# Performance work log

Measured on AMD Instinct MI355X. Metric: run time of the kernel, lower is better.

The kernel has to match this reference:

```python
import jax, jax.numpy as jnp
import numpy as np

H = 16; KV = 4; D = 128; HID = 2048; MAX_POS = 4096; RANK = 8; ALPHA = 16.0; THETA = 10000.0


def _lora_dense(x, kernel, a, b):
    # base kernel path is stop-gradient'd in the original LoRADense
    x = x.astype(jnp.bfloat16)
    y = x @ jax.lax.stop_gradient(kernel.astype(jnp.bfloat16))
    y = y + (ALPHA / RANK) * ((x @ a.astype(jnp.bfloat16)) @ b.astype(jnp.bfloat16))
    return y.astype(jnp.float32)


def _apply_rope(xq, xk, position_ids):
    # complex rotation expressed with real cos/sin on interleaved (even, odd) pairs
    dt = xq.dtype
    xq = xq.astype(jnp.bfloat16).astype(jnp.float32)
    xk = xk.astype(jnp.bfloat16).astype(jnp.float32)
    d = xq.shape[-1]
    inv_freq = 1.0 / THETA ** (jnp.arange(0, d, 2)[: d // 2].astype(jnp.float32) / d)
    angles = jnp.arange(MAX_POS, dtype=jnp.float32)[:, None] * inv_freq[None, :]  # (max_pos, d/2)
    cos = jnp.cos(angles)[position_ids][:, :, None, :]  # (b, s, 1, d/2)
    sin = jnp.sin(angles)[position_ids][:, :, None, :]

    def rot(x):
        xe = x[..., 0::2]
        xo = x[..., 1::2]
        re = xe * cos - xo * sin
        im = xe * sin + xo * cos
        return jnp.stack((re, im), axis=-1).reshape(x.shape)

    return rot(xq).astype(dt), rot(xk).astype(dt)


def _forward(hidden_states, attention_mask, position_ids, wq_kernel, wq_a, wq_b,
             wk_kernel, wk_a, wk_b, wv_kernel, wv_a, wv_b, wo_kernel, wo_a, wo_b):
    b, s, _ = hidden_states.shape
    hs = hidden_states.astype(jnp.bfloat16)
    xq = _lora_dense(hs, wq_kernel, wq_a, wq_b).reshape(b, s, H, D)
    g = H // KV
    # GQA: repeat each kv head g times along the head axis ('b s (h d) -> b s (h g) d')
    xk = jnp.repeat(_lora_dense(hs, wk_kernel, wk_a, wk_b).reshape(b, s, KV, D), g, axis=2)
    xv = jnp.repeat(_lora_dense(hs, wv_kernel, wv_a, wv_b).reshape(b, s, KV, D), g, axis=2)
    xq, xk = _apply_rope(xq, xk, position_ids)
    causal = jnp.tril(jnp.ones((s, s), dtype=bool))
    mask = attention_mask[:, None, None, :] & causal[None, None]  # (b, 1, q, k)
    bias = jnp.where(mask, 0.0, jnp.finfo(jnp.float32).min)
    scale = 1.0 / np.sqrt(D).astype(np.float32)
    scores = jnp.einsum('bqhd,bkhd->bhqk', (xq * scale).astype(jnp.bfloat16),
                        xk.astype(jnp.bfloat16)).astype(jnp.float32) + bias
    attn = jax.nn.softmax(scores, axis=-1)
    out = jnp.einsum('bhqk,bkhd->bqhd', attn, xv).reshape(b, s, H * D)
    return _lora_dense(out, wo_kernel, wo_a, wo_b)


def setup_inputs():
    key = jax.random.key(0)
    ks = jax.random.split(key, 16)
    B, S = 2, 2048
    w = lambda k, shp, sc=0.02: jax.random.normal(k, shp, dtype=jnp.float32) * sc
    return {
        'hidden_states': jax.random.normal(ks[0], (B, S, HID), dtype=jnp.float32),
        'attention_mask': jnp.ones((B, S), dtype=bool),
        'position_ids': jnp.broadcast_to(jnp.arange(S, dtype=jnp.int32), (B, S)),
        'wq_kernel': w(ks[1], (HID, H * D)),
        'wq_a': w(ks[2], (HID, RANK), 0.01),
        'wq_b': w(ks[3], (RANK, H * D), 0.01),
        'wk_kernel': w(ks[4], (HID, KV * D)),
        'wk_a': w(ks[5], (HID, RANK), 0.01),
        'wk_b': w(ks[6], (RANK, KV * D), 0.01),
        'wv_kernel': w(ks[7], (HID, KV * D)),
        'wv_a': w(ks[8], (HID, RANK), 0.01),
        'wv_b': w(ks[9], (RANK, KV * D), 0.01),
        'wo_kernel': w(ks[10], (H * D, HID)),
        'wo_a': w(ks[11], (H * D, RANK), 0.01),
        'wo_b': w(ks[12], (RANK, HID), 0.01),
    }


def reference(hidden_states, attention_mask, position_ids, wq_kernel, wq_a, wq_b,
              wk_kernel, wk_a, wk_b, wv_kernel, wv_a, wv_b, wo_kernel, wo_a, wo_b):
    return _forward(hidden_states, attention_mask, position_ids, wq_kernel, wq_a, wq_b,
                    wk_kernel, wk_a, wk_b, wv_kernel, wv_a, wv_b, wo_kernel, wo_a, wo_b)
```

## Files before the change

### kernel.cpp

```cpp
#include <hip/hip_runtime.h>
#include <hip/hip_bf16.h>
#include <cstdint>

#define H_    16
#define KV_   4
#define D_    128
#define HID_  2048
#define B_    2
#define S_    2048
#define NROW_ (B_*S_)
#define HD_   (H_*D_)
#define KVD_  (KV_*D_)
#define NQKV_ (HD_ + 2*KVD_)
#define SCALE_ 0.08838834764831843f
#define L2E_   1.44269504088896f
#define QSC_   (SCALE_ * L2E_)
#define THR2_  11.5415603f
#define NEG_  -1e30f

typedef float  f32x4  __attribute__((ext_vector_type(4)));
typedef __bf16 bf16x8 __attribute__((ext_vector_type(8)));
typedef __bf16 bf16x4 __attribute__((ext_vector_type(4)));

__device__ __forceinline__ unsigned short f2bf(float x) {
  unsigned u = __float_as_uint(x);
  return (unsigned short)((u + 0x7FFFu + ((u >> 16) & 1u)) >> 16);
}
__device__ __forceinline__ float bf2f(unsigned short h) {
  return __uint_as_float(((unsigned)h) << 16);
}

__device__ __forceinline__ void glds16(const void* g, void* l) {
  typedef __attribute__((address_space(1))) const char G;
  typedef __attribute__((address_space(3))) char L;
  __builtin_amdgcn_global_load_lds((const G*)(unsigned long long)g,
                                   (L*)(unsigned)(unsigned long long)l, 16, 0, 0);
}

__global__ __launch_bounds__(256) void fold_all(
    const float* __restrict__ wq, const float* __restrict__ wqa, const float* __restrict__ wqb,
    const float* __restrict__ wk, const float* __restrict__ wka, const float* __restrict__ wkb,
    const float* __restrict__ wv, const float* __restrict__ wva, const float* __restrict__ wvb,
    const float* __restrict__ wo, const float* __restrict__ woa, const float* __restrict__ wob,
    unsigned short* __restrict__ Wqkv, unsigned short* __restrict__ Wot,
    const float* __restrict__ hs, unsigned short* __restrict__ Xb,
    float* __restrict__ tab) {
  const int z = blockIdx.z;
  const int tid = threadIdx.x;
  if (z == 4) {
    int lin = blockIdx.y * 32 + blockIdx.x;
    size_t base = (size_t)lin * 2048 + tid * 8;
#pragma unroll
    for (int i = 0; i < 8; ++i) {
      float4 v = ((const float4*)hs)[base + i];
      ushort4 o; o.x = f2bf(v.x); o.y = f2bf(v.y); o.z = f2bf(v.z); o.w = f2bf(v.w);
      ((ushort4*)Xb)[base + i] = o;
    }
    return;
  }
  if (z == 5) {
    int lin = blockIdx.y * 32 + blockIdx.x;
    if (lin >= 512) return;
    int p = lin * 4 + (tid >> 6);
    int j = tid & 63;
    float invf = __powf(10000.0f, -(float)j / 64.0f);
    float a = (float)p * invf;
    float s, c;
    sincosf(a, &s, &c);
    tab[(p * 64 + j) * 2 + 0] = c;
    tab[(p * 64 + j) * 2 + 1] = s;
    return;
  }
  const float *W, *A, *Bm; unsigned short* Wt; int N;
  if (z == 0)      { W = wq; A = wqa; Bm = wqb; Wt = Wqkv;                         N = 2048; }
  else if (z == 1) { W = wk; A = wka; Bm = wkb; Wt = Wqkv + (size_t)2048 * 2048;   N = 512;  }
  else if (z == 2) { W = wv; A = wva; Bm = wvb; Wt = Wqkv + (size_t)2560 * 2048;   N = 512;  }
  else             { W = wo; A = woa; Bm = wob; Wt = Wot;                          N = 2048; }
  const int K = 2048;
  const int k0 = blockIdx.x << 6, n0 = blockIdx.y << 6;
  if (n0 >= N) return;

  __shared__ float Bs[8 * 64];
  __shared__ unsigned short tt[64 * 72];
#pragma unroll
  for (int i = 0; i < 2; ++i) {
    int c = i * 256 + tid;
    Bs[c] = bf2f(f2bf(Bm[(c >> 6) * N + n0 + (c & 63)]));
  }
  __syncthreads();
  const int kr = tid >> 2, nc = (tid & 3) << 4;
  float a[8];
#pragma unroll
  for (int r = 0; r < 8; ++r) a[r] = 2.0f * bf2f(f2bf(A[(k0 + kr) * 8 + r]));
#pragma unroll
  for (int i = 0; i < 4; ++i) {
    float4 wv4 = *(const float4*)(W + (size_t)(k0 + kr) * N + n0 + nc + i * 4);
    float e[4] = {wv4.x, wv4.y, wv4.z, wv4.w};
#pragma unroll
    for (int q = 0; q < 4; ++q) {
      int n = nc + i * 4 + q;
      float acc = bf2f(f2bf(e[q]));
#pragma unroll
      for (int r = 0; r < 8; ++r) acc += a[r] * Bs[r * 64 + n];
      tt[kr * 72 + n] = f2bf(acc);
    }
  }
  __syncthreads();
  const int nr = tid >> 2, kc = (tid & 3) << 4;
#pragma unroll
  for (int i = 0; i < 2; ++i) {
    unsigned short o[8];
#pragma unroll
    for (int e2 = 0; e2 < 8; ++e2) o[e2] = tt[(kc + i * 8 + e2) * 72 + nr];
    *(bf16x8*)(Wt + (size_t)(n0 + nr) * K + k0 + kc + i * 8) = *(const bf16x8*)o;
  }
}

__global__ __launch_bounds__(256) void ropevt(unsigned short* __restrict__ QKV,
                                              const int* __restrict__ pos,
                                              const float* __restrict__ trig,
                                              unsigned short* __restrict__ VT) {
  __shared__ unsigned short t[64 * 65];
  const int bx = blockIdx.x, tid = threadIdx.x;
  if (bx < 2560) {
    int gid = bx * 256 + tid;
    int row = gid / 160;
    int ch = gid - row * 160;
    bool isq = ch < 128;
    int col = isq ? (ch << 4) : (HD_ + ((ch - 128) << 4));
    int j0 = (isq ? (ch & 7) : ((ch - 128) & 7)) << 3;
    int pp = pos[row];
    const float* tb = trig + ((size_t)pp * 64 + j0) * 2;
    float4 t0 = *(const float4*)(tb);
    float4 t1 = *(const float4*)(tb + 4);
    float4 t2 = *(const float4*)(tb + 8);
    float4 t3 = *(const float4*)(tb + 12);
    float cc[8] = {t0.x, t0.z, t1.x, t1.z, t2.x, t2.z, t3.x, t3.z};
    float ss[8] = {t0.y, t0.w, t1.y, t1.w, t2.y, t2.w, t3.y, t3.w};
    unsigned short* base = QKV + (size_t)row * NQKV_ + col;
    unsigned short xin[16], xo[16];
    *(bf16x8*)xin = *(const bf16x8*)base;
    *(bf16x8*)(xin + 8) = *(const bf16x8*)(base + 8);
    float scl = isq ? QSC_ : 1.0f;
#pragma unroll
    for (int p = 0; p < 8; ++p) {
      float x0 = bf2f(xin[2 * p]), x1 = bf2f(xin[2 * p + 1]);
      float re = (x0 * cc[p] - x1 * ss[p]) * scl;
      float im = (x0 * ss[p] + x1 * cc[p]) * scl;
      xo[2 * p] = f2bf(re); xo[2 * p + 1] = f2bf(im);
    }
    *(bf16x8*)base = *(const bf16x8*)xo;
    *(bf16x8*)(base + 8) = *(const bf16x8*)(xo + 8);
  } else {
    const int bb = bx - 2560;
    const int s0 = (bb & 31) << 6, d0 = ((bb >> 5) & 1) << 6;
    const int bk = bb >> 6, b = bk >> 2, hkv = bk & 3;
#pragma unroll
    for (int i = 0; i < 2; ++i) {
      int c = i * 256 + tid;
      int sr = c >> 3, c8 = c & 7;
      bf16x8 v = *(const bf16x8*)(QKV + (size_t)(b * S_ + s0 + sr) * NQKV_
                                  + HD_ + KVD_ + hkv * D_ + d0 + c8 * 8);
      const unsigned short* u = (const unsigned short*)&v;
#pragma unroll
      for (int k = 0; k < 8; ++k) t[sr * 65 + c8 * 8 + k] = u[k];
    }
    __syncthreads();
#pragma unroll
    for (int i = 0; i < 2; ++i) {
      int c = i * 256 + tid;
      int dr = c >> 3, c8 = c & 7;
      unsigned short o[8];
#pragma unroll
      for (int k = 0; k < 8; ++k) o[k] = t[(c8 * 8 + k) * 65 + dr];
      *(bf16x8*)(VT + ((size_t)(bk * 128 + d0 + dr)) * S_ + s0 + c8 * 8) =
          *(const bf16x8*)o;
    }
  }
}

template <int BN, int OUTF32>
__global__ __launch_bounds__(512, 1) void gemm8p(const unsigned short* __restrict__ A,
                                                 const unsigned short* __restrict__ Bt,
                                                 void* __restrict__ C,
                                                 int M, int N, int K) {
  constexpr int ASLAB = 256 * 64;
  constexpr int BSLAB = BN * 64;
  constexpr int NFR = BN / 64;
  constexpr int WCOL = BN / 4;
  __shared__ __align__(16) unsigned short lds[3 * ASLAB + 2 * BSLAB];
  unsigned short* const ldsB = lds + 3 * ASLAB;
  const int tid = threadIdx.x, lane = tid & 63, w = tid >> 6;
  const int g = lane >> 4, l15 = lane & 15;
  const int wm = w >> 2, wn = w & 3;

  const int x = blockIdx.x & 7, inner = blockIdx.x >> 3;
  const int bm = (x >> 1) * 4 + (inner >> 3);
  const int bn = (x & 1) * 8 + (inner & 7);
  const int row0 = bm << 8, col0 = bn * BN;
  const int nkt = K >> 6;

  auto stA = [&](int kt, int slab, int part) {
    if (kt < nkt) {
#pragma unroll
      for (int j = 0; j < 2; ++j) {
        int jj = part * 2 + j;
        int c = jj * 512 + tid;
        int r = c >> 3, s = c & 7, slot = s ^ (r & 7);
        glds16(A + (size_t)(row0 + r) * K + (kt << 6) + slot * 8,
               (char*)(lds + slab * ASLAB) + (size_t)(jj * 512 + w * 64) * 16);
      }
    }
  };
  auto stB = [&](int kt, int slab, int part) {
    if (kt < nkt) {
      constexpr int split = (NFR == 3) ? 2 : 1;
      const int jlo = part ? split : 0;
      const int jhi = part ? NFR : split;
#pragma unroll
      for (int jj = 0; jj < NFR; ++jj) {
        if (jj >= jlo && jj < jhi) {
          int c = jj * 512 + tid;
          int r = c >> 3, s = c & 7, slot = s ^ (r & 7);
          glds16(Bt + (size_t)(col0 + r) * K + (kt << 6) + slot * 8,
                 (char*)(ldsB + slab * BSLAB) + (size_t)(jj * 512 + w * 64) * 16);
        }
      }
    }
  };

  f32x4 acc[8][NFR];
#pragma unroll
  for (int i = 0; i < 8; ++i)
#pragma unroll
    for (int j = 0; j < NFR; ++j) acc[i][j] = (f32x4){0.f, 0.f, 0.f, 0.f};
  bf16x8 bfr[NFR][2];

  stB(0, 0, 0); stB(0, 0, 1);
  stA(0, 0, 0); stA(0, 0, 1);
  stA(1, 1, 0); stA(1, 1, 1);
  asm volatile("s_waitcnt vmcnt(0)" ::: "memory");
  __builtin_amdgcn_s_barrier();

  int am = 0;
  for (int kt = 0; kt < nkt; ++kt) {
    const unsigned short* bufA = lds + am * ASLAB;
    const unsigned short* bufB = ldsB + (kt & 1) * BSLAB;
    int as2 = am + 2; if (as2 >= 3) as2 -= 3;
    const int bs1 = (kt + 1) & 1;
#pragma unroll
    for (int q = 0; q < 4; ++q) {
      bf16x8 af[2][2];
#pragma unroll
      for (int mi = 0; mi < 2; ++mi) {
        int r = wm * 128 + q * 32 + mi * 16 + l15;
#pragma unroll
        for (int ks = 0; ks < 2; ++ks) {
          int slot = (ks * 4 + g) ^ (r & 7);
          af[mi][ks] = *(const bf16x8*)(bufA + r * 64 + slot * 8);
        }
      }
      if (q == 0) {
#pragma unroll
        for (int ni = 0; ni < NFR; ++ni) {
          int r = wn * WCOL + ni * 16 + l15;
#pragma unroll
          for (int ks = 0; ks < 2; ++ks) {
            int slot = (ks * 4 + g) ^ (r & 7);
            bfr[ni][ks] = *(const bf16x8*)(bufB + r * 64 + slot * 8);
          }
        }
      }
      if (q == 0)      stB(kt + 1, bs1, 0);
      else if (q == 1) stB(kt + 1, bs1, 1);
      else if (q == 2) stA(kt + 2, as2, 0);
      else {
        stA(kt + 2, as2, 1);
        if (kt + 2 < nkt) asm volatile("s_waitcnt vmcnt(4)" ::: "memory");
        else              asm volatile("s_waitcnt vmcnt(0)" ::: "memory");
      }
      __builtin_amdgcn_s_barrier();
      asm volatile("s_waitcnt lgkmcnt(0)" ::: "memory");
      __builtin_amdgcn_s_setprio(1);
#pragma unroll
      for (int ks = 0; ks < 2; ++ks)
#pragma unroll
        for (int mi = 0; mi < 2; ++mi)
#pragma unroll
          for (int ni = 0; ni < NFR; ++ni)
            acc[q * 2 + mi][ni] =
                __builtin_amdgcn_mfma_f32_16x16x32_bf16(af[mi][ks], bfr[ni][ks],
                                                        acc[q * 2 + mi][ni], 0, 0, 0);
      __builtin_amdgcn_s_setprio(0);
      __builtin_amdgcn_s_barrier();
    }
    am = (am + 1 == 3) ? 0 : am + 1;
  }

#pragma unroll
  for (int f = 0; f < 8; ++f)
#pragma unroll
    for (int jj = 0; jj < 4; ++jj) {
      int r = row0 + wm * 128 + f * 16 + g * 4 + jj;
#pragma unroll
      for (int ni = 0; ni < NFR; ++ni) {
        int cc = col0 + wn * WCOL + ni * 16 + l15;
        float v = acc[f][ni][jj];
        if (OUTF32) ((float*)C)[(size_t)r * N + cc] = v;
        else        ((unsigned short*)C)[(size_t)r * N + cc] = f2bf(v);
      }
    }
}

__global__ __launch_bounds__(512, 4) void attn_k(const unsigned short* __restrict__ QKV,
                                                 const unsigned short* __restrict__ VT,
                                                 unsigned short* __restrict__ O) {
  __shared__ __align__(16) unsigned short smem[32768];
  const int tid = threadIdx.x, lane = tid & 63, w = tid >> 6;
  const int g = lane >> 4, l15 = lane & 15;
  const int wr = w & 1;
  const int wh = w >> 1;

  const int dd = blockIdx.x;
  const int grp = dd & 7;
  const int b = grp >> 2, hkv = grp & 3;
  const int qt = 63 - (dd >> 3);
  const int q_base = qt << 5;
  const int ntile = (qt >> 1) + 1;
  const int h = hkv * 4 + wh;

  const unsigned short* QKVk0 = QKV + (size_t)b * S_ * NQKV_ + HD_ + hkv * D_;
  const unsigned short* VT0  = VT + (size_t)(b * 4 + hkv) * 128 * S_;

  int gk[2], gv[2], dsl[2];
#pragma unroll
  for (int i = 0; i < 2; ++i) {
    int c = i * 512 + tid;
    { int r = c >> 4, s = c & 15; gk[i] = r * NQKV_ + (s ^ (r & 7)) * 8; }
    { int d = c >> 3, s = c & 7;  gv[i] = d * S_ + (s ^ (d & 7)) * 8; }
    dsl[i] = (i * 512 + w * 64) * 16;
  }
  int koff[4][4], voff[2][8], pwo[4], pro[2];
#pragma unroll
  for (int ks = 0; ks < 4; ++ks)
#pragma unroll
    for (int m = 0; m < 4; ++m) {
      int r = m * 16 + l15;
      koff[ks][m] = r * 128 + ((ks * 4 + g) ^ (r & 7)) * 8;
    }
#pragma unroll
  for (int ks = 0; ks < 2; ++ks)
#pragma unroll
    for (int nd = 0; nd < 8; ++nd) {
      int d = nd * 16 + l15;
      voff[ks][nd] = d * 64 + ((ks * 4 + g) ^ (d & 7)) * 8;
    }
#pragma unroll
  for (int m = 0; m < 4; ++m)
    pwo[m] = l15 * 64 + ((2 * m + (g >> 1) + l15) & 7) * 8 + (g & 1) * 4;
#pragma unroll
  for (int ks = 0; ks < 2; ++ks)
    pro[ks] = l15 * 64 + ((ks * 4 + g + l15) & 7) * 8;
  const int PB = 24576 + w * 1024;
  char* const smemc = (char*)smem;
  const int qg = q_base + wr * 16 + l15;

#define STAGEKV(KB, VOB) do {                                               \
    const unsigned short* bk_ = QKVk0 + (size_t)(KB) * NQKV_;               \
    const unsigned short* bv_ = VT0 + (KB);                                 \
    _Pragma("unroll")                                                       \
    for (int i_ = 0; i_ < 2; ++i_) {                                        \
      glds16(bk_ + gk[i_], smemc + dsl[i_]);                                \
      glds16(bv_ + gv[i_], smemc + (VOB) + dsl[i_]);                        \
    }                                                                       \
  } while (0)

#define QKT(SACC) do {                                                      \
    _Pragma("unroll") for (int m = 0; m < 4; ++m)                           \
      SACC[m] = (f32x4){0.f, 0.f, 0.f, 0.f};                                \
    __builtin_amdgcn_s_setprio(1);                                          \
    _Pragma("unroll") for (int ks = 0; ks < 4; ++ks) {                      \
      bf16x8 kf[4];                                                         \
      _Pragma("unroll") for (int m = 0; m < 4; ++m)                         \
        kf[m] = *(const bf16x8*)(smem + koff[ks][m]);                       \
      _Pragma("unroll") for (int m = 0; m < 4; ++m)                         \
        SACC[m] = __builtin_amdgcn_mfma_f32_16x16x32_bf16(kf[m], qf[ks], SACC[m], 0, 0, 0); \
    }                                                                       \
    __builtin_amdgcn_s_setprio(0);                                          \
  } while (0)

#define SOFTPV(SACC, VOHS, TCUR) do {                                       \
    if ((TCUR) == ntile - 1) {                                              \
      const int kb_ = (TCUR) << 6;                                          \
      _Pragma("unroll") for (int m = 0; m < 4; ++m)                         \
        _Pragma("unroll") for (int jj = 0; jj < 4; ++jj)                    \
          if (kb_ + m * 16 + g * 4 + jj > qg) SACC[m][jj] = NEG_;           \
    }                                                                       \
    float pm = NEG_;                                                        \
    _Pragma("unroll") for (int m = 0; m < 4; ++m)                           \
      _Pragma("unroll") for (int jj = 0; jj < 4; ++jj)                      \
        pm = fmaxf(pm, SACC[m][jj]);                                        \
    bool skip = __all(pm <= mrun + THR2_);                                  \
    float mnew;                                                             \
    if (skip) {                                                             \
      mnew = mrun;                                                          \
    } else {                                                                \
      pm = fmaxf(pm, __shfl_xor(pm, 16));                                   \
      pm = fmaxf(pm, __shfl_xor(pm, 32));                                   \
      mnew = fmaxf(mrun, pm);                                               \
    }                                                                       \
    float ls = 0.f;                                                         \
    _Pragma("unroll") for (int m = 0; m < 4; ++m)                           \
      _Pragma("unroll") for (int jj = 0; jj < 4; ++jj) {                    \
        float pv = __builtin_amdgcn_exp2f(SACC[m][jj] - mnew);              \
        SACC[m][jj] = pv;                                                   \
        ls += pv;                                                           \
      }                                                                     \
    _Pragma("unroll") for (int m = 0; m < 4; ++m) {                         \
      bf16x4 pk = {(__bf16)SACC[m][0], (__bf16)SACC[m][1],                  \
                   (__bf16)SACC[m][2], (__bf16)SACC[m][3]};                 \
      *(bf16x4*)(smem + PB + pwo[m]) = pk;                                  \
    }                                                                       \
    if (skip) {                                                             \
      lrun += ls;                                                           \
    } else {                                                                \
      float sc = __builtin_amdgcn_exp2f(mrun - mnew);                       \
      lrun = lrun * sc + ls;                                                \
      mrun = mnew;                                                          \
      _Pragma("unroll") for (int jj = 0; jj < 4; ++jj) {                    \
        int srcl = (lane & 48) | (g * 4 + jj);                              \
        float s = __shfl(sc, srcl);                                         \
        _Pragma("unroll") for (int nd = 0; nd < 8; ++nd) oacc[nd][jj] *= s; \
      }                                                                     \
    }                                                                       \
    __builtin_amdgcn_s_setprio(1);                                          \
    _Pragma("unroll") for (int ks = 0; ks < 2; ++ks) {                      \
      bf16x8 pf = *(const bf16x8*)(smem + PB + pro[ks]);                    \
      _Pragma("unroll") for (int nd = 0; nd < 8; ++nd) {                    \
        bf16x8 vf = *(const bf16x8*)(smem + (VOHS) + voff[ks][nd]);         \
        oacc[nd] = __builtin_amdgcn_mfma_f32_16x16x32_bf16(pf, vf, oacc[nd], 0, 0, 0); \
      }                                                                     \
    }                                                                       \
    __builtin_amdgcn_s_setprio(0);                                          \
  } while (0)

  bf16x8 qf[4];
#pragma unroll
  for (int ks = 0; ks < 4; ++ks)
    qf[ks] = *(const bf16x8*)(QKV + (size_t)(b * S_ + qg) * NQKV_
                              + h * D_ + ks * 32 + g * 8);

  f32x4 oacc[8];
#pragma unroll
  for (int nd = 0; nd < 8; ++nd) oacc[nd] = (f32x4){0.f, 0.f, 0.f, 0.f};
  float mrun = NEG_, lrun = 0.f;

  STAGEKV(0, 16384);
  __syncthreads();
  for (int t = 0; t < ntile; t += 2) {
    {
      f32x4 sacc[4];
      QKT(sacc);
      __syncthreads();
      if (t + 1 < ntile) STAGEKV((t + 1) << 6, 32768);
      SOFTPV(sacc, 8192, t);
      __syncthreads();
    }
    if (t + 1 >= ntile) break;
    {
      f32x4 sacc[4];
      QKT(sacc);
      __syncthreads();
      if (t + 2 < ntile) STAGEKV((t + 2) << 6, 16384);
      SOFTPV(sacc, 16384, t + 1);
      __syncthreads();
    }
  }

  lrun += __shfl_xor(lrun, 16);
  lrun += __shfl_xor(lrun, 32);

  float inv[4];
#pragma unroll
  for (int jj = 0; jj < 4; ++jj) {
    int srcl = (lane & 48) | (g * 4 + jj);
    inv[jj] = 1.0f / __shfl(lrun, srcl);
  }
  unsigned short* sE = smem + wh * 4352;
#pragma unroll
  for (int nd = 0; nd < 8; ++nd)
#pragma unroll
    for (int jj = 0; jj < 4; ++jj) {
      __bf16 e = (__bf16)(oacc[nd][jj] * inv[jj]);
      sE[(wr * 16 + g * 4 + jj) * 136 + nd * 16 + l15] = *(unsigned short*)&e;
    }
  __syncthreads();
#pragma unroll
  for (int i = 0; i < 4; ++i) {
    int c = i * 512 + tid;
    int hh2 = c >> 9, r = (c >> 4) & 31, c16 = c & 15;
    bf16x8 vv = *(const bf16x8*)(smem + hh2 * 4352 + r * 136 + c16 * 8);
    *(bf16x8*)(O + (size_t)(b * S_ + q_base + r) * HD_ + (hkv * 4 + hh2) * D_ + c16 * 8) = vv;
  }
#undef STAGEKV
#undef QKT
#undef SOFTPV
}

extern "C" void kernel_launch(void* const* d_in, const int* in_sizes, int n_in,
                              void* d_out, int out_size, void* d_ws, size_t ws_size,
                              hipStream_t stream) {
  const float* hs  = (const float*)d_in[0];
  const int*   pos = (const int*)d_in[2];
  const float* wq  = (const float*)d_in[3];
  const float* wqa = (const float*)d_in[4];
  const float* wqb = (const float*)d_in[5];
  const float* wk  = (const float*)d_in[6];
  const float* wka = (const float*)d_in[7];
  const float* wkb = (const float*)d_in[8];
  const float* wv  = (const float*)d_in[9];
  const float* wva = (const float*)d_in[10];
  const float* wvb = (const float*)d_in[11];
  const float* wo  = (const float*)d_in[12];
  const float* woa = (const float*)d_in[13];
  const float* wob = (const float*)d_in[14];

  char* ws = (char*)d_ws;
  unsigned short* Xb   = (unsigned short*)(ws);
  unsigned short* Wqkv = (unsigned short*)(ws + 16777216);
  unsigned short* Wot  = (unsigned short*)(ws + 29360128);
  unsigned short* QKV  = (unsigned short*)(ws + 37748736);
  unsigned short* VT   = (unsigned short*)(ws + 62914560);
  float*          trig = (float*)(ws + 67108864);

  fold_all<<<dim3(32, 32, 6), 256, 0, stream>>>(wq, wqa, wqb, wk, wka, wkb,
                                                wv, wva, wvb, wo, woa, wob,
                                                Wqkv, Wot, hs, Xb, trig);
  gemm8p<192, 0><<<256, 512, 0, stream>>>(Xb, Wqkv, QKV, 4096, 3072, 2048);
  ropevt<<<3072, 256, 0, stream>>>(QKV, pos, trig, VT);
  attn_k<<<512, 512, 0, stream>>>(QKV, VT, Xb );
  gemm8p<128, 1><<<256, 512, 0, stream>>>(Xb, Wot, d_out, 4096, 2048, 2048);
}
```

Baseline: 189.0 us.

## Give each attention wave two 16-row query slabs to reuse K/V fragments

The attention kernel drops from 8 waves per block to 4. Each wave now handles one head and both 16-row query sub-tiles, so every K and V fragment read from shared memory feeds two MFMAs instead of one. The main loop is restructured to process one tile per iteration with alternating buffers, and per-row softmax state is doubled. This cuts LDS read traffic per MFMA, at the cost of more registers per thread and fewer waves to hide latency.

```diff
diff --git a/kernel.cpp b/kernel.cpp
--- a/kernel.cpp
+++ b/kernel.cpp
@@ -312,14 +312,12 @@
     }
 }
 
-__global__ __launch_bounds__(512, 4) void attn_k(const unsigned short* __restrict__ QKV,
+__global__ __launch_bounds__(256, 2) void attn_k(const unsigned short* __restrict__ QKV,
                                                  const unsigned short* __restrict__ VT,
                                                  unsigned short* __restrict__ O) {
   __shared__ __align__(16) unsigned short smem[32768];
   const int tid = threadIdx.x, lane = tid & 63, w = tid >> 6;
   const int g = lane >> 4, l15 = lane & 15;
-  const int wr = w & 1;
-  const int wh = w >> 1;
 
   const int dd = blockIdx.x;
   const int grp = dd & 7;
@@ -327,20 +325,20 @@
   const int qt = 63 - (dd >> 3);
   const int q_base = qt << 5;
   const int ntile = (qt >> 1) + 1;
-  const int h = hkv * 4 + wh;
+  const int h = hkv * 4 + w;
 
   const unsigned short* QKVk0 = QKV + (size_t)b * S_ * NQKV_ + HD_ + hkv * D_;
   const unsigned short* VT0  = VT + (size_t)(b * 4 + hkv) * 128 * S_;
 
-  int gk[2], gv[2], dsl[2];
-#pragma unroll
-  for (int i = 0; i < 2; ++i) {
-    int c = i * 512 + tid;
+  int gk[4], gv[4], dsl[4];
+#pragma unroll
+  for (int i = 0; i < 4; ++i) {
+    int c = i * 256 + tid;
     { int r = c >> 4, s = c & 15; gk[i] = r * NQKV_ + (s ^ (r & 7)) * 8; }
     { int d = c >> 3, s = c & 7;  gv[i] = d * S_ + (s ^ (d & 7)) * 8; }
-    dsl[i] = (i * 512 + w * 64) * 16;
-  }
-  int koff[4][4], voff[2][8], pwo[4], pro[2];
+    dsl[i] = (i * 256 + w * 64) * 16;
+  }
+  int koff[4][4], voff[2][8], pwo[2][4], pro[2][2];
 #pragma unroll
   for (int ks = 0; ks < 4; ++ks)
 #pragma unroll
@@ -356,155 +354,178 @@
       voff[ks][nd] = d * 64 + ((ks * 4 + g) ^ (d & 7)) * 8;
     }
 #pragma unroll
-  for (int m = 0; m < 4; ++m)
-    pwo[m] = l15 * 64 + ((2 * m + (g >> 1) + l15) & 7) * 8 + (g & 1) * 4;
-#pragma unroll
-  for (int ks = 0; ks < 2; ++ks)
-    pro[ks] = l15 * 64 + ((ks * 4 + g + l15) & 7) * 8;
-  const int PB = 24576 + w * 1024;
+  for (int n = 0; n < 2; ++n)
+#pragma unroll
+    for (int m = 0; m < 4; ++m)
+      pwo[n][m] = (n * 16 + l15) * 64 + ((2 * m + (g >> 1) + l15) & 7) * 8 + (g & 1) * 4;
+#pragma unroll
+  for (int mq = 0; mq < 2; ++mq)
+#pragma unroll
+    for (int ks = 0; ks < 2; ++ks)
+      pro[mq][ks] = (mq * 16 + l15) * 64 + ((ks * 4 + g + l15) & 7) * 8;
+  const int PB = 24576 + w * 2048;
   char* const smemc = (char*)smem;
-  const int qg = q_base + wr * 16 + l15;
 
 #define STAGEKV(KB, VOB) do {                                               \
     const unsigned short* bk_ = QKVk0 + (size_t)(KB) * NQKV_;               \
     const unsigned short* bv_ = VT0 + (KB);                                 \
     _Pragma("unroll")                                                       \
-    for (int i_ = 0; i_ < 2; ++i_) {                                        \
+    for (int i_ = 0; i_ < 4; ++i_) {                                        \
       glds16(bk_ + gk[i_], smemc + dsl[i_]);                                \
       glds16(bv_ + gv[i_], smemc + (VOB) + dsl[i_]);                        \
     }                                                                       \
   } while (0)
 
-#define QKT(SACC) do {                                                      \
-    _Pragma("unroll") for (int m = 0; m < 4; ++m)                           \
-      SACC[m] = (f32x4){0.f, 0.f, 0.f, 0.f};                                \
-    __builtin_amdgcn_s_setprio(1);                                          \
-    _Pragma("unroll") for (int ks = 0; ks < 4; ++ks) {                      \
-      bf16x8 kf[4];                                                         \
-      _Pragma("unroll") for (int m = 0; m < 4; ++m)                         \
-        kf[m] = *(const bf16x8*)(smem + koff[ks][m]);                       \
-      _Pragma("unroll") for (int m = 0; m < 4; ++m)                         \
-        SACC[m] = __builtin_amdgcn_mfma_f32_16x16x32_bf16(kf[m], qf[ks], SACC[m], 0, 0, 0); \
-    }                                                                       \
-    __builtin_amdgcn_s_setprio(0);                                          \
-  } while (0)
-
-#define SOFTPV(SACC, VOHS, TCUR) do {                                       \
-    if ((TCUR) == ntile - 1) {                                              \
-      const int kb_ = (TCUR) << 6;                                          \
-      _Pragma("unroll") for (int m = 0; m < 4; ++m)                         \
-        _Pragma("unroll") for (int jj = 0; jj < 4; ++jj)                    \
-          if (kb_ + m * 16 + g * 4 + jj > qg) SACC[m][jj] = NEG_;           \
-    }                                                                       \
-    float pm = NEG_;                                                        \
-    _Pragma("unroll") for (int m = 0; m < 4; ++m)                           \
-      _Pragma("unroll") for (int jj = 0; jj < 4; ++jj)                      \
-        pm = fmaxf(pm, SACC[m][jj]);                                        \
-    bool skip = __all(pm <= mrun + THR2_);                                  \
-    float mnew;                                                             \
-    if (skip) {                                                             \
-      mnew = mrun;                                                          \
-    } else {                                                                \
-      pm = fmaxf(pm, __shfl_xor(pm, 16));                                   \
-      pm = fmaxf(pm, __shfl_xor(pm, 32));                                   \
-      mnew = fmaxf(mrun, pm);                                               \
-    }                                                                       \
-    float ls = 0.f;                                                         \
-    _Pragma("unroll") for (int m = 0; m < 4; ++m)                           \
-      _Pragma("unroll") for (int jj = 0; jj < 4; ++jj) {                    \
-        float pv = __builtin_amdgcn_exp2f(SACC[m][jj] - mnew);              \
-        SACC[m][jj] = pv;                                                   \
-        ls += pv;                                                           \
-      }                                                                     \
-    _Pragma("unroll") for (int m = 0; m < 4; ++m) {                         \
-      bf16x4 pk = {(__bf16)SACC[m][0], (__bf16)SACC[m][1],                  \
-                   (__bf16)SACC[m][2], (__bf16)SACC[m][3]};                 \
-      *(bf16x4*)(smem + PB + pwo[m]) = pk;                                  \
-    }                                                                       \
-    if (skip) {                                                             \
-      lrun += ls;                                                           \
-    } else {                                                                \
-      float sc = __builtin_amdgcn_exp2f(mrun - mnew);                       \
-      lrun = lrun * sc + ls;                                                \
-      mrun = mnew;                                                          \
-      _Pragma("unroll") for (int jj = 0; jj < 4; ++jj) {                    \
-        int srcl = (lane & 48) | (g * 4 + jj);                              \
-        float s = __shfl(sc, srcl);                                         \
-        _Pragma("unroll") for (int nd = 0; nd < 8; ++nd) oacc[nd][jj] *= s; \
-      }                                                                     \
-    }                                                                       \
-    __builtin_amdgcn_s_setprio(1);                                          \
-    _Pragma("unroll") for (int ks = 0; ks < 2; ++ks) {                      \
-      bf16x8 pf = *(const bf16x8*)(smem + PB + pro[ks]);                    \
-      _Pragma("unroll") for (int nd = 0; nd < 8; ++nd) {                    \
-        bf16x8 vf = *(const bf16x8*)(smem + (VOHS) + voff[ks][nd]);         \
-        oacc[nd] = __builtin_amdgcn_mfma_f32_16x16x32_bf16(pf, vf, oacc[nd], 0, 0, 0); \
-      }                                                                     \
-    }                                                                       \
-    __builtin_amdgcn_s_setprio(0);                                          \
-  } while (0)
-
-  bf16x8 qf[4];
-#pragma unroll
-  for (int ks = 0; ks < 4; ++ks)
-    qf[ks] = *(const bf16x8*)(QKV + (size_t)(b * S_ + qg) * NQKV_
-                              + h * D_ + ks * 32 + g * 8);
-
-  f32x4 oacc[8];
-#pragma unroll
-  for (int nd = 0; nd < 8; ++nd) oacc[nd] = (f32x4){0.f, 0.f, 0.f, 0.f};
-  float mrun = NEG_, lrun = 0.f;
+  bf16x8 qf[2][4];
+#pragma unroll
+  for (int n = 0; n < 2; ++n)
+#pragma unroll
+    for (int ks = 0; ks < 4; ++ks)
+      qf[n][ks] = *(const bf16x8*)(QKV + (size_t)(b * S_ + q_base + n * 16 + l15) * NQKV_
+                                   + h * D_ + ks * 32 + g * 8);
+
+  f32x4 oacc[2][8];
+#pragma unroll
+  for (int n = 0; n < 2; ++n)
+#pragma unroll
+    for (int nd = 0; nd < 8; ++nd) oacc[n][nd] = (f32x4){0.f, 0.f, 0.f, 0.f};
+  float mrun[2] = {NEG_, NEG_}, lrun[2] = {0.f, 0.f};
 
   STAGEKV(0, 16384);
   __syncthreads();
-  for (int t = 0; t < ntile; t += 2) {
-    {
-      f32x4 sacc[4];
-      QKT(sacc);
-      __syncthreads();
-      if (t + 1 < ntile) STAGEKV((t + 1) << 6, 32768);
-      SOFTPV(sacc, 8192, t);
-      __syncthreads();
-    }
-    if (t + 1 >= ntile) break;
-    {
-      f32x4 sacc[4];
-      QKT(sacc);
-      __syncthreads();
-      if (t + 2 < ntile) STAGEKV((t + 2) << 6, 16384);
-      SOFTPV(sacc, 16384, t + 1);
-      __syncthreads();
-    }
-  }
-
-  lrun += __shfl_xor(lrun, 16);
-  lrun += __shfl_xor(lrun, 32);
-
-  float inv[4];
-#pragma unroll
-  for (int jj = 0; jj < 4; ++jj) {
-    int srcl = (lane & 48) | (g * 4 + jj);
-    inv[jj] = 1.0f / __shfl(lrun, srcl);
-  }
-  unsigned short* sE = smem + wh * 4352;
-#pragma unroll
-  for (int nd = 0; nd < 8; ++nd)
+  for (int t = 0; t < ntile; ++t) {
+    const int vcur = 8192 + (t & 1) * 8192;
+    f32x4 sacc[4][2];
+#pragma unroll
+    for (int m = 0; m < 4; ++m)
+#pragma unroll
+      for (int n = 0; n < 2; ++n) sacc[m][n] = (f32x4){0.f, 0.f, 0.f, 0.f};
+    __builtin_amdgcn_s_setprio(1);
+#pragma unroll
+    for (int ks = 0; ks < 4; ++ks) {
+      bf16x8 kf[4];
+#pragma unroll
+      for (int m = 0; m < 4; ++m)
+        kf[m] = *(const bf16x8*)(smem + koff[ks][m]);
+#pragma unroll
+      for (int m = 0; m < 4; ++m)
+#pragma unroll
+        for (int n = 0; n < 2; ++n)
+          sacc[m][n] = __builtin_amdgcn_mfma_f32_16x16x32_bf16(kf[m], qf[n][ks], sacc[m][n], 0, 0, 0);
+    }
+    __builtin_amdgcn_s_setprio(0);
+    __syncthreads();
+    if (t + 1 < ntile) STAGEKV((t + 1) << 6, 16384 + ((t + 1) & 1) * 16384);
+
+    if (t == ntile - 1) {
+      const int kb_ = t << 6;
+#pragma unroll
+      for (int m = 0; m < 4; ++m)
+#pragma unroll
+        for (int n = 0; n < 2; ++n)
+#pragma unroll
+          for (int jj = 0; jj < 4; ++jj)
+            if (kb_ + m * 16 + g * 4 + jj > q_base + n * 16 + l15)
+              sacc[m][n][jj] = NEG_;
+    }
+#pragma unroll
+    for (int n = 0; n < 2; ++n) {
+      float pm = NEG_;
+#pragma unroll
+      for (int m = 0; m < 4; ++m)
+#pragma unroll
+        for (int jj = 0; jj < 4; ++jj) pm = fmaxf(pm, sacc[m][n][jj]);
+      bool skip = __all(pm <= mrun[n] + THR2_);
+      float mnew;
+      if (skip) {
+        mnew = mrun[n];
+      } else {
+        pm = fmaxf(pm, __shfl_xor(pm, 16));
+        pm = fmaxf(pm, __shfl_xor(pm, 32));
+        mnew = fmaxf(mrun[n], pm);
+      }
+      float ls = 0.f;
+#pragma unroll
+      for (int m = 0; m < 4; ++m)
+#pragma unroll
+        for (int jj = 0; jj < 4; ++jj) {
+          float pv = __builtin_amdgcn_exp2f(sacc[m][n][jj] - mnew);
+          sacc[m][n][jj] = pv;
+          ls += pv;
+        }
+#pragma unroll
+      for (int m = 0; m < 4; ++m) {
+        bf16x4 pk = {(__bf16)sacc[m][n][0], (__bf16)sacc[m][n][1],
+                     (__bf16)sacc[m][n][2], (__bf16)sacc[m][n][3]};
+        *(bf16x4*)(smem + PB + pwo[n][m]) = pk;
+      }
+      if (skip) {
+        lrun[n] += ls;
+      } else {
+        float sc = __builtin_amdgcn_exp2f(mrun[n] - mnew);
+        lrun[n] = lrun[n] * sc + ls;
+        mrun[n] = mnew;
+#pragma unroll
+        for (int jj = 0; jj < 4; ++jj) {
+          int srcl = (lane & 48) | (g * 4 + jj);
+          float s = __shfl(sc, srcl);
+#pragma unroll
+          for (int nd = 0; nd < 8; ++nd) oacc[n][nd][jj] *= s;
+        }
+      }
+    }
+
+    __builtin_amdgcn_s_setprio(1);
+#pragma unroll
+    for (int ks = 0; ks < 2; ++ks) {
+      bf16x8 pf[2];
+#pragma unroll
+      for (int mq = 0; mq < 2; ++mq)
+        pf[mq] = *(const bf16x8*)(smem + PB + pro[mq][ks]);
+#pragma unroll
+      for (int nd = 0; nd < 8; ++nd) {
+        bf16x8 vf = *(const bf16x8*)(smem + vcur + voff[ks][nd]);
+#pragma unroll
+        for (int mq = 0; mq < 2; ++mq)
+          oacc[mq][nd] = __builtin_amdgcn_mfma_f32_16x16x32_bf16(pf[mq], vf, oacc[mq][nd], 0, 0, 0);
+      }
+    }
+    __builtin_amdgcn_s_setprio(0);
+    __syncthreads();
+  }
+
+#pragma unroll
+  for (int n = 0; n < 2; ++n) {
+    lrun[n] += __shfl_xor(lrun[n], 16);
+    lrun[n] += __shfl_xor(lrun[n], 32);
+  }
+  float inv[2][4];
+#pragma unroll
+  for (int n = 0; n < 2; ++n)
 #pragma unroll
     for (int jj = 0; jj < 4; ++jj) {
-      __bf16 e = (__bf16)(oacc[nd][jj] * inv[jj]);
-      sE[(wr * 16 + g * 4 + jj) * 136 + nd * 16 + l15] = *(unsigned short*)&e;
-    }
+      int srcl = (lane & 48) | (g * 4 + jj);
+      inv[n][jj] = 1.0f / __shfl(lrun[n], srcl);
+    }
+  unsigned short* sE = smem + w * 4352;
+#pragma unroll
+  for (int n = 0; n < 2; ++n)
+#pragma unroll
+    for (int nd = 0; nd < 8; ++nd)
+#pragma unroll
+      for (int jj = 0; jj < 4; ++jj) {
+        __bf16 e = (__bf16)(oacc[n][nd][jj] * inv[n][jj]);
+        sE[(n * 16 + g * 4 + jj) * 136 + nd * 16 + l15] = *(unsigned short*)&e;
+      }
   __syncthreads();
 #pragma unroll
-  for (int i = 0; i < 4; ++i) {
-    int c = i * 512 + tid;
+  for (int i = 0; i < 8; ++i) {
+    int c = i * 256 + tid;
     int hh2 = c >> 9, r = (c >> 4) & 31, c16 = c & 15;
     bf16x8 vv = *(const bf16x8*)(smem + hh2 * 4352 + r * 136 + c16 * 8);
     *(bf16x8*)(O + (size_t)(b * S_ + q_base + r) * HD_ + (hkv * 4 + hh2) * D_ + c16 * 8) = vv;
   }
 #undef STAGEKV
-#undef QKT
-#undef SOFTPV
 }
 
 extern "C" void kernel_launch(void* const* d_in, const int* in_sizes, int n_in,
@@ -538,6 +559,6 @@
                                                 Wqkv, Wot, hs, Xb, trig);
   gemm8p<192, 0><<<256, 512, 0, stream>>>(Xb, Wqkv, QKV, 4096, 3072, 2048);
   ropevt<<<3072, 256, 0, stream>>>(QKV, pos, trig, VT);
-  attn_k<<<512, 512, 0, stream>>>(QKV, VT, Xb );
+  attn_k<<<512, 256, 0, stream>>>(QKV, VT, Xb );
   gemm8p<128, 1><<<256, 512, 0, stream>>>(Xb, Wot, d_out, 4096, 2048, 2048);
 }
```

Measured after the change: 186.4 us. About the same (-1.4%).
